# Kernel tuning notes

Measured on AMD Instinct MI355X. Metric: run time of the kernel, lower is better.

Reference implementation:

```python
import jax, jax.numpy as jnp
import numpy as np

N = 100000      # nodes
E = 1000000     # edges (avg degree ~10)
IN_DIM = 128
OUT_DIM = 64
NEG_SLOPE = 0.2  # GATLayerST alpha


def setup_inputs() -> dict:
    key = jax.random.key(0)
    k1, k2, k3, k4, k5 = jax.random.split(key, 5)
    X = jax.random.normal(k1, (N, IN_DIM), dtype=jnp.float32)
    edge_index = jax.random.randint(k2, (2, E), 0, N, dtype=jnp.int64)
    W = jax.random.normal(k3, (IN_DIM, OUT_DIM), dtype=jnp.float32) * 0.05
    a_l = jax.random.normal(k4, (OUT_DIM,), dtype=jnp.float32) * 0.05
    a_r = jax.random.normal(k5, (OUT_DIM,), dtype=jnp.float32) * 0.05
    return {"X": X, "edge_index": edge_index, "W": W, "a_l": a_l, "a_r": a_r}


def reference(X, edge_index, W, a_l, a_r):
    # Single-head GAT (nhead=1, concat irrelevant), no residual/activation/norm,
    # dropout disabled (inference). edge_weight unused by attention path.
    src = edge_index[0]
    dst = edge_index[1]

    h = X @ W                          # [N, OUT]
    el = h @ a_l                       # [N] source-side attention term
    er = h @ a_r                       # [N] destination-side attention term

    # per-edge logits
    e = jax.nn.leaky_relu(el[src] + er[dst], negative_slope=NEG_SLOPE)  # [E]

    # segment softmax over incoming edges of each destination node
    e_max = jax.ops.segment_max(e, dst, num_segments=N)
    e_max = jnp.where(jnp.isfinite(e_max), e_max, jnp.zeros_like(e_max))
    e_exp = jnp.exp(e - e_max[dst])                                     # [E]
    denom = jax.ops.segment_sum(e_exp, dst, num_segments=N)            # [N]
    alpha = e_exp / jnp.maximum(denom[dst], 1e-16)                      # [E]

    # weighted scatter-add aggregation
    out = jax.ops.segment_sum(alpha[:, None] * h[src], dst, num_segments=N)  # [N, OUT]
    return out
```

## Files before the change

### kernel.cpp

```cpp
#include <hip/hip_runtime.h>
#include <math.h>

#define IN_DIM 128
#define OUT_DIM 64
#define NEG_SLOPE 0.2f

#define ROWS_PER_WAVE 8
#define ROWS_PER_BLOCK 32

#define SCAN_ITEMS 4
#define SCAN_BLOCK 1024
#define SCAN_CHUNK (SCAN_BLOCK * SCAN_ITEMS)

__global__ __launch_bounds__(256) void gemm_kernel(
        const float* __restrict__ X, const float* __restrict__ W,
        const float* __restrict__ a_l, const float* __restrict__ a_r,
        float* __restrict__ h, float* __restrict__ el, float* __restrict__ er, int n)
{
    __shared__ float Wl[IN_DIM * OUT_DIM];
    __shared__ float Xl[4][ROWS_PER_WAVE * IN_DIM];
    const int tid  = threadIdx.x;
    const int wave = tid >> 6;
    const int lane = tid & 63;

    {
        const float4* W4  = (const float4*)W;
        float4*       Wl4 = (float4*)Wl;
        #pragma unroll
        for (int i = 0; i < 8; ++i)
            Wl4[i * 256 + tid] = W4[i * 256 + tid];
    }

    const int row0 = blockIdx.x * ROWS_PER_BLOCK + wave * ROWS_PER_WAVE;

    if (row0 + ROWS_PER_WAVE <= n) {
        const float4* Xs = (const float4*)(X + (size_t)row0 * IN_DIM);
        float4*       Xd = (float4*)Xl[wave];
        #pragma unroll
        for (int i = 0; i < 4; ++i)
            Xd[i * 64 + lane] = Xs[i * 64 + lane];
    } else if (row0 < n) {
        for (int r = 0; r < ROWS_PER_WAVE; ++r) {
            if (row0 + r < n) {
                float2 v = ((const float2*)(X + (size_t)(row0 + r) * IN_DIM))[lane];
                Xl[wave][r * IN_DIM + lane * 2]     = v.x;
                Xl[wave][r * IN_DIM + lane * 2 + 1] = v.y;
            }
        }
    }
    __syncthreads();
    if (row0 >= n) return;

    float acc[ROWS_PER_WAVE] = {};
    const float* Xw = Xl[wave];
    #pragma unroll 2
    for (int kq = 0; kq < IN_DIM / 4; ++kq) {
        const int k = kq * 4;
        const float w0 = Wl[(k    ) * OUT_DIM + lane];
        const float w1 = Wl[(k + 1) * OUT_DIM + lane];
        const float w2 = Wl[(k + 2) * OUT_DIM + lane];
        const float w3 = Wl[(k + 3) * OUT_DIM + lane];
        #pragma unroll
        for (int r = 0; r < ROWS_PER_WAVE; ++r) {
            const float4 x = *(const float4*)(Xw + r * IN_DIM + k);
            acc[r] = fmaf(x.x, w0, acc[r]);
            acc[r] = fmaf(x.y, w1, acc[r]);
            acc[r] = fmaf(x.z, w2, acc[r]);
            acc[r] = fmaf(x.w, w3, acc[r]);
        }
    }

    const float alv = a_l[lane];
    const float arv = a_r[lane];
    #pragma unroll
    for (int r = 0; r < ROWS_PER_WAVE; ++r) {
        const int row = row0 + r;
        if (row >= n) break;
        h[(size_t)row * OUT_DIM + lane] = acc[r];
        float vl = acc[r] * alv;
        float vr = acc[r] * arv;
        #pragma unroll
        for (int off = 32; off > 0; off >>= 1) {
            vl += __shfl_xor(vl, off);
            vr += __shfl_xor(vr, off);
        }
        if (lane == 0) { el[row] = vl; er[row] = vr; }
    }
}

__global__ void degree_rank_kernel(const int* __restrict__ dst, int* __restrict__ deg,
                                   int* __restrict__ erank, int e) {
    int i = blockIdx.x * blockDim.x + threadIdx.x;
    if (i < e) erank[i] = atomicAdd(&deg[dst[i]], 1);
}

__global__ __launch_bounds__(SCAN_BLOCK) void scan_partials_kernel(
        const int* __restrict__ deg, int* __restrict__ bsum, int n)
{
    __shared__ int wsum[SCAN_BLOCK / 64];
    const int tid  = threadIdx.x;
    const int lane = tid & 63;
    const int wave = tid >> 6;
    const int base = blockIdx.x * SCAN_CHUNK + tid * SCAN_ITEMS;

    int s = 0;
    if (base + SCAN_ITEMS <= n) {
        int4 v = *(const int4*)(deg + base);
        s = v.x + v.y + v.z + v.w;
    } else {
        for (int i = 0; i < SCAN_ITEMS; ++i)
            if (base + i < n) s += deg[base + i];
    }
    #pragma unroll
    for (int off = 32; off > 0; off >>= 1) s += __shfl_xor(s, off);
    if (lane == 0) wsum[wave] = s;
    __syncthreads();
    if (tid == 0) {
        int t = 0;
        #pragma unroll
        for (int i = 0; i < SCAN_BLOCK / 64; ++i) t += wsum[i];
        bsum[blockIdx.x] = t;
    }
}

__global__ __launch_bounds__(64) void scan_bsum_kernel(int* __restrict__ bsum, int nb) {
    const int t = threadIdx.x;
    int orig = (t < nb) ? bsum[t] : 0;
    int v = orig;
    #pragma unroll
    for (int off = 1; off < 64; off <<= 1) {
        int u = __shfl_up(v, off);
        if (t >= off) v += u;
    }
    if (t < nb) bsum[t] = v - orig;
}

__global__ __launch_bounds__(SCAN_BLOCK) void scan_apply_kernel(
        const int* __restrict__ deg, const int* __restrict__ bsum,
        int* __restrict__ offsets, int n, int e)
{
    __shared__ int wsum[SCAN_BLOCK / 64];
    const int tid  = threadIdx.x;
    const int lane = tid & 63;
    const int wave = tid >> 6;
    const int base = blockIdx.x * SCAN_CHUNK + tid * SCAN_ITEMS;

    int v[SCAN_ITEMS];
    if (base + SCAN_ITEMS <= n) {
        int4 t4 = *(const int4*)(deg + base);
        v[0] = t4.x; v[1] = t4.y; v[2] = t4.z; v[3] = t4.w;
    } else {
        #pragma unroll
        for (int i = 0; i < SCAN_ITEMS; ++i)
            v[i] = (base + i < n) ? deg[base + i] : 0;
    }
    int s = 0;
    #pragma unroll
    for (int i = 0; i < SCAN_ITEMS; ++i) s += v[i];

    int incl = s;
    #pragma unroll
    for (int off = 1; off < 64; off <<= 1) {
        int u = __shfl_up(incl, off);
        if (lane >= off) incl += u;
    }
    if (lane == 63) wsum[wave] = incl;
    __syncthreads();
    if (wave == 0 && lane < SCAN_BLOCK / 64) {
        int ws = wsum[lane];
        int wv = ws;
        #pragma unroll
        for (int off = 1; off < SCAN_BLOCK / 64; off <<= 1) {
            int u = __shfl_up(wv, off);
            if (lane >= off) wv += u;
        }
        wsum[lane] = wv - ws;
    }
    __syncthreads();

    int run = bsum[blockIdx.x] + wsum[wave] + (incl - s);
    #pragma unroll
    for (int i = 0; i < SCAN_ITEMS; ++i) {
        int idx = base + i;
        if (idx < n) {
            offsets[idx] = run;
            run += v[i];
        }
    }
    if (blockIdx.x == 0 && tid == 0) offsets[n] = e;
}

__global__ void scatter_kernel(
        const int* __restrict__ src, const int* __restrict__ dst,
        const int* __restrict__ offsets, const int* __restrict__ erank,
        int* __restrict__ esrc, int e)
{
    int i = blockIdx.x * blockDim.x + threadIdx.x;
    if (i >= e) return;
    esrc[offsets[dst[i]] + erank[i]] = src[i];
}

__global__ __launch_bounds__(256) void gat_node_kernel(
        const int* __restrict__ esrc, const int* __restrict__ offsets,
        const float* __restrict__ el, const float* __restrict__ er,
        const float* __restrict__ h, float* __restrict__ out, int n)
{
    const int node = blockIdx.x * 4 + (threadIdx.x >> 6);
    const int lane = threadIdx.x & 63;
    if (node >= n) return;

    const int start = offsets[node];
    const int deg   = offsets[node + 1] - start;

    float acc = 0.f;
    if (deg > 0) {
        const float erd = er[node];
        if (deg <= 64) {
            int   s = 0;
            float x = -INFINITY;
            if (lane < deg) {
                s = esrc[start + lane];
                x = el[s] + erd;
                x = (x > 0.f) ? x : NEG_SLOPE * x;
            }
            float m = x;
            #pragma unroll
            for (int off = 32; off > 0; off >>= 1) m = fmaxf(m, __shfl_xor(m, off));
            float ex = (lane < deg) ? __expf(x - m) : 0.f;
            float dsum = ex;
            #pragma unroll
            for (int off = 32; off > 0; off >>= 1) dsum += __shfl_xor(dsum, off);
            const float a = ex * (1.f / dsum);

            float acc0 = 0.f, acc1 = 0.f, acc2 = 0.f, acc3 = 0.f;
            int j = 0;
            for (; j + 4 <= deg; j += 4) {
                const float a0 = __shfl(a, j),     a1 = __shfl(a, j + 1);
                const float a2 = __shfl(a, j + 2), a3 = __shfl(a, j + 3);
                const int   s0 = __shfl(s, j),     s1 = __shfl(s, j + 1);
                const int   s2 = __shfl(s, j + 2), s3 = __shfl(s, j + 3);
                const float h0 = h[(size_t)s0 * OUT_DIM + lane];
                const float h1 = h[(size_t)s1 * OUT_DIM + lane];
                const float h2 = h[(size_t)s2 * OUT_DIM + lane];
                const float h3 = h[(size_t)s3 * OUT_DIM + lane];
                acc0 = fmaf(a0, h0, acc0);
                acc1 = fmaf(a1, h1, acc1);
                acc2 = fmaf(a2, h2, acc2);
                acc3 = fmaf(a3, h3, acc3);
            }
            for (; j < deg; ++j) {
                const float aj = __shfl(a, j);
                const int   sj = __shfl(s, j);
                acc0 = fmaf(aj, h[(size_t)sj * OUT_DIM + lane], acc0);
            }
            acc = (acc0 + acc1) + (acc2 + acc3);
        } else {
            float m = -INFINITY;
            for (int base = 0; base < deg; base += 64) {
                int idx = base + lane;
                if (idx < deg) {
                    int ss = esrc[start + idx];
                    float xx = el[ss] + erd;
                    xx = (xx > 0.f) ? xx : NEG_SLOPE * xx;
                    m = fmaxf(m, xx);
                }
            }
            #pragma unroll
            for (int off = 32; off > 0; off >>= 1) m = fmaxf(m, __shfl_xor(m, off));

            float dsum = 0.f;
            for (int base = 0; base < deg; base += 64) {
                int idx = base + lane;
                if (idx < deg) {
                    int ss = esrc[start + idx];
                    float xx = el[ss] + erd;
                    xx = (xx > 0.f) ? xx : NEG_SLOPE * xx;
                    dsum += __expf(xx - m);
                }
            }
            #pragma unroll
            for (int off = 32; off > 0; off >>= 1) dsum += __shfl_xor(dsum, off);
            const float inv = 1.f / dsum;

            float acc0 = 0.f, acc1 = 0.f, acc2 = 0.f, acc3 = 0.f;
            for (int base = 0; base < deg; base += 64) {
                int idx = base + lane;
                int   ss = 0;
                float av = 0.f;
                if (idx < deg) {
                    ss = esrc[start + idx];
                    float xx = el[ss] + erd;
                    xx = (xx > 0.f) ? xx : NEG_SLOPE * xx;
                    av = __expf(xx - m) * inv;
                }
                const int cnt = min(64, deg - base);
                int j = 0;
                for (; j + 4 <= cnt; j += 4) {
                    const float a0 = __shfl(av, j),     a1 = __shfl(av, j + 1);
                    const float a2 = __shfl(av, j + 2), a3 = __shfl(av, j + 3);
                    const int   s0 = __shfl(ss, j),     s1 = __shfl(ss, j + 1);
                    const int   s2 = __shfl(ss, j + 2), s3 = __shfl(ss, j + 3);
                    acc0 = fmaf(a0, h[(size_t)s0 * OUT_DIM + lane], acc0);
                    acc1 = fmaf(a1, h[(size_t)s1 * OUT_DIM + lane], acc1);
                    acc2 = fmaf(a2, h[(size_t)s2 * OUT_DIM + lane], acc2);
                    acc3 = fmaf(a3, h[(size_t)s3 * OUT_DIM + lane], acc3);
                }
                for (; j < cnt; ++j) {
                    const float aj = __shfl(av, j);
                    const int   sj = __shfl(ss, j);
                    acc0 = fmaf(aj, h[(size_t)sj * OUT_DIM + lane], acc0);
                }
            }
            acc = (acc0 + acc1) + (acc2 + acc3);
        }
    }
    out[(size_t)node * OUT_DIM + lane] = acc;
}

extern "C" void kernel_launch(void* const* d_in, const int* in_sizes, int n_in,
                              void* d_out, int out_size, void* d_ws, size_t ws_size,
                              hipStream_t stream) {
    const float* X   = (const float*)d_in[0];
    const int*   ei  = (const int*)  d_in[1];
    const float* W   = (const float*)d_in[2];
    const float* a_l = (const float*)d_in[3];
    const float* a_r = (const float*)d_in[4];
    float* out = (float*)d_out;

    const int n = in_sizes[0] / IN_DIM;
    const int e = in_sizes[1] / 2;
    const int* src = ei;
    const int* dst = ei + e;

    char* ws = (char*)d_ws;
    auto carve = [&](size_t bytes) {
        char* p = ws;
        ws += (bytes + 255) & ~(size_t)255;
        return p;
    };
    float* h       = (float*)carve((size_t)n * OUT_DIM * sizeof(float));
    float* el      = (float*)carve((size_t)n * sizeof(float));
    float* er      = (float*)carve((size_t)n * sizeof(float));
    int*   deg     = (int*)  carve((size_t)n * sizeof(int));
    int*   offsets = (int*)  carve((size_t)(n + 1) * sizeof(int));
    int*   erank   = (int*)  carve((size_t)e * sizeof(int));
    int*   esrc    = (int*)  carve((size_t)e * sizeof(int));
    int*   bsum    = (int*)  carve(64 * sizeof(int));

    const int nscan = (n + SCAN_CHUNK - 1) / SCAN_CHUNK;

    hipMemsetAsync(deg, 0, (size_t)n * sizeof(int), stream);
    gemm_kernel<<<(n + ROWS_PER_BLOCK - 1) / ROWS_PER_BLOCK, 256, 0, stream>>>(
        X, W, a_l, a_r, h, el, er, n);
    degree_rank_kernel<<<(e + 255) / 256, 256, 0, stream>>>(dst, deg, erank, e);
    scan_partials_kernel<<<nscan, SCAN_BLOCK, 0, stream>>>(deg, bsum, n);
    scan_bsum_kernel<<<1, 64, 0, stream>>>(bsum, nscan);
    scan_apply_kernel<<<nscan, SCAN_BLOCK, 0, stream>>>(deg, bsum, offsets, n, e);
    scatter_kernel<<<(e + 255) / 256, 256, 0, stream>>>(src, dst, offsets, erank, esrc, e);
    gat_node_kernel<<<(n + 3) / 4, 256, 0, stream>>>(esrc, offsets, el, er, h, out, n);
}
```

Measured before the change: 260.3 us.

## Store h in bf16 and read X directly from global in GEMM

Stores the intermediate projected features h as bfloat16 instead of fp32, which halves the bytes of the random h[src] gathers in the aggregation kernel and of the h write. The GEMM kernel also stops staging X in shared memory. Each wave now reads its X rows straight from global memory with a wave-uniform row index. The bf16 rounding adds error to the aggregated output and may approach tolerance limits.

```diff
diff --git a/kernel.cpp b/kernel.cpp
--- a/kernel.cpp
+++ b/kernel.cpp
@@ -1,4 +1,5 @@
 #include <hip/hip_runtime.h>
+#include <hip/hip_bf16.h>
 #include <math.h>
 
 #define IN_DIM 128
@@ -15,13 +16,13 @@
 __global__ __launch_bounds__(256) void gemm_kernel(
         const float* __restrict__ X, const float* __restrict__ W,
         const float* __restrict__ a_l, const float* __restrict__ a_r,
-        float* __restrict__ h, float* __restrict__ el, float* __restrict__ er, int n)
+        __hip_bfloat16* __restrict__ h, float* __restrict__ el, float* __restrict__ er,
+        int n)
 {
     __shared__ float Wl[IN_DIM * OUT_DIM];
-    __shared__ float Xl[4][ROWS_PER_WAVE * IN_DIM];
     const int tid  = threadIdx.x;
-    const int wave = tid >> 6;
     const int lane = tid & 63;
+    const int wv = __builtin_amdgcn_readfirstlane(tid >> 6);
 
     {
         const float4* W4  = (const float4*)W;
@@ -30,43 +31,37 @@
         for (int i = 0; i < 8; ++i)
             Wl4[i * 256 + tid] = W4[i * 256 + tid];
     }
-
-    const int row0 = blockIdx.x * ROWS_PER_BLOCK + wave * ROWS_PER_WAVE;
-
+    __syncthreads();
+
+    const int row0 = blockIdx.x * ROWS_PER_BLOCK + wv * ROWS_PER_WAVE;
+    if (row0 >= n) return;
+    const float* __restrict__ Xr = X + (size_t)row0 * IN_DIM;
+
+    float acc[ROWS_PER_WAVE] = {};
     if (row0 + ROWS_PER_WAVE <= n) {
-        const float4* Xs = (const float4*)(X + (size_t)row0 * IN_DIM);
-        float4*       Xd = (float4*)Xl[wave];
-        #pragma unroll
-        for (int i = 0; i < 4; ++i)
-            Xd[i * 64 + lane] = Xs[i * 64 + lane];
-    } else if (row0 < n) {
+        #pragma unroll 2
+        for (int kq = 0; kq < IN_DIM / 4; ++kq) {
+            const int k = kq * 4;
+            const float w0 = Wl[(k    ) * OUT_DIM + lane];
+            const float w1 = Wl[(k + 1) * OUT_DIM + lane];
+            const float w2 = Wl[(k + 2) * OUT_DIM + lane];
+            const float w3 = Wl[(k + 3) * OUT_DIM + lane];
+            #pragma unroll
+            for (int r = 0; r < ROWS_PER_WAVE; ++r) {
+                const float4 x = *(const float4*)(Xr + r * IN_DIM + k);
+                acc[r] = fmaf(x.x, w0, acc[r]);
+                acc[r] = fmaf(x.y, w1, acc[r]);
+                acc[r] = fmaf(x.z, w2, acc[r]);
+                acc[r] = fmaf(x.w, w3, acc[r]);
+            }
+        }
+    } else {
         for (int r = 0; r < ROWS_PER_WAVE; ++r) {
-            if (row0 + r < n) {
-                float2 v = ((const float2*)(X + (size_t)(row0 + r) * IN_DIM))[lane];
-                Xl[wave][r * IN_DIM + lane * 2]     = v.x;
-                Xl[wave][r * IN_DIM + lane * 2 + 1] = v.y;
-            }
-        }
-    }
-    __syncthreads();
-    if (row0 >= n) return;
-
-    float acc[ROWS_PER_WAVE] = {};
-    const float* Xw = Xl[wave];
-    #pragma unroll 2
-    for (int kq = 0; kq < IN_DIM / 4; ++kq) {
-        const int k = kq * 4;
-        const float w0 = Wl[(k    ) * OUT_DIM + lane];
-        const float w1 = Wl[(k + 1) * OUT_DIM + lane];
-        const float w2 = Wl[(k + 2) * OUT_DIM + lane];
-        const float w3 = Wl[(k + 3) * OUT_DIM + lane];
-        #pragma unroll
-        for (int r = 0; r < ROWS_PER_WAVE; ++r) {
-            const float4 x = *(const float4*)(Xw + r * IN_DIM + k);
-            acc[r] = fmaf(x.x, w0, acc[r]);
-            acc[r] = fmaf(x.y, w1, acc[r]);
-            acc[r] = fmaf(x.z, w2, acc[r]);
-            acc[r] = fmaf(x.w, w3, acc[r]);
+            if (row0 + r >= n) break;
+            float a = 0.f;
+            for (int k = 0; k < IN_DIM; ++k)
+                a = fmaf(Xr[r * IN_DIM + k], Wl[k * OUT_DIM + lane], a);
+            acc[r] = a;
         }
     }
 
@@ -76,7 +71,7 @@
     for (int r = 0; r < ROWS_PER_WAVE; ++r) {
         const int row = row0 + r;
         if (row >= n) break;
-        h[(size_t)row * OUT_DIM + lane] = acc[r];
+        h[(size_t)row * OUT_DIM + lane] = __float2bfloat16(acc[r]);
         float vl = acc[r] * alv;
         float vr = acc[r] * arv;
         #pragma unroll
@@ -203,7 +198,7 @@
 __global__ __launch_bounds__(256) void gat_node_kernel(
         const int* __restrict__ esrc, const int* __restrict__ offsets,
         const float* __restrict__ el, const float* __restrict__ er,
-        const float* __restrict__ h, float* __restrict__ out, int n)
+        const __hip_bfloat16* __restrict__ h, float* __restrict__ out, int n)
 {
     const int node = blockIdx.x * 4 + (threadIdx.x >> 6);
     const int lane = threadIdx.x & 63;
@@ -239,10 +234,10 @@
                 const float a2 = __shfl(a, j + 2), a3 = __shfl(a, j + 3);
                 const int   s0 = __shfl(s, j),     s1 = __shfl(s, j + 1);
                 const int   s2 = __shfl(s, j + 2), s3 = __shfl(s, j + 3);
-                const float h0 = h[(size_t)s0 * OUT_DIM + lane];
-                const float h1 = h[(size_t)s1 * OUT_DIM + lane];
-                const float h2 = h[(size_t)s2 * OUT_DIM + lane];
-                const float h3 = h[(size_t)s3 * OUT_DIM + lane];
+                const float h0 = __bfloat162float(h[(size_t)s0 * OUT_DIM + lane]);
+                const float h1 = __bfloat162float(h[(size_t)s1 * OUT_DIM + lane]);
+                const float h2 = __bfloat162float(h[(size_t)s2 * OUT_DIM + lane]);
+                const float h3 = __bfloat162float(h[(size_t)s3 * OUT_DIM + lane]);
                 acc0 = fmaf(a0, h0, acc0);
                 acc1 = fmaf(a1, h1, acc1);
                 acc2 = fmaf(a2, h2, acc2);
@@ -251,7 +246,7 @@
             for (; j < deg; ++j) {
                 const float aj = __shfl(a, j);
                 const int   sj = __shfl(s, j);
-                acc0 = fmaf(aj, h[(size_t)sj * OUT_DIM + lane], acc0);
+                acc0 = fmaf(aj, __bfloat162float(h[(size_t)sj * OUT_DIM + lane]), acc0);
             }
             acc = (acc0 + acc1) + (acc2 + acc3);
         } else {
@@ -300,15 +295,15 @@
                     const float a2 = __shfl(av, j + 2), a3 = __shfl(av, j + 3);
                     const int   s0 = __shfl(ss, j),     s1 = __shfl(ss, j + 1);
                     const int   s2 = __shfl(ss, j + 2), s3 = __shfl(ss, j + 3);
-                    acc0 = fmaf(a0, h[(size_t)s0 * OUT_DIM + lane], acc0);
-                    acc1 = fmaf(a1, h[(size_t)s1 * OUT_DIM + lane], acc1);
-                    acc2 = fmaf(a2, h[(size_t)s2 * OUT_DIM + lane], acc2);
-                    acc3 = fmaf(a3, h[(size_t)s3 * OUT_DIM + lane], acc3);
+                    acc0 = fmaf(a0, __bfloat162float(h[(size_t)s0 * OUT_DIM + lane]), acc0);
+                    acc1 = fmaf(a1, __bfloat162float(h[(size_t)s1 * OUT_DIM + lane]), acc1);
+                    acc2 = fmaf(a2, __bfloat162float(h[(size_t)s2 * OUT_DIM + lane]), acc2);
+                    acc3 = fmaf(a3, __bfloat162float(h[(size_t)s3 * OUT_DIM + lane]), acc3);
                 }
                 for (; j < cnt; ++j) {
                     const float aj = __shfl(av, j);
                     const int   sj = __shfl(ss, j);
-                    acc0 = fmaf(aj, h[(size_t)sj * OUT_DIM + lane], acc0);
+                    acc0 = fmaf(aj, __bfloat162float(h[(size_t)sj * OUT_DIM + lane]), acc0);
                 }
             }
             acc = (acc0 + acc1) + (acc2 + acc3);
@@ -338,7 +333,7 @@
         ws += (bytes + 255) & ~(size_t)255;
         return p;
     };
-    float* h       = (float*)carve((size_t)n * OUT_DIM * sizeof(float));
+    __hip_bfloat16* h = (__hip_bfloat16*)carve((size_t)n * OUT_DIM * sizeof(__hip_bfloat16));
     float* el      = (float*)carve((size_t)n * sizeof(float));
     float* er      = (float*)carve((size_t)n * sizeof(float));
     int*   deg     = (int*)  carve((size_t)n * sizeof(int));
```

New measurement: 271.9 us. 4.4% more time.
